# Performance work log

Hardware: AMD Instinct MI355X
Metric: run time of the kernel (lower is better)

Reference implementation:

```python
import jax, jax.numpy as jnp
import numpy as np

DIM = 768
HEADS = 12
HEAD_DIM = DIM // HEADS
TOPK = 100
SCALE = HEAD_DIM ** -0.5


def setup_inputs() -> dict:
    key = jax.random.key(0)
    k1, k2, k3, k4 = jax.random.split(key, 4)
    B, N = 8, 1024
    x = jax.random.normal(k1, (B, N, DIM), dtype=jnp.float32)
    # torch nn.Linear(dim, 3*dim, bias=False): store matmul-ready [in, out]
    w_qkv = jax.random.normal(k2, (DIM, 3 * DIM), dtype=jnp.float32) * (DIM ** -0.5)
    w_proj = jax.random.normal(k3, (DIM, DIM), dtype=jnp.float32) * (DIM ** -0.5)
    b_proj = jax.random.normal(k4, (DIM,), dtype=jnp.float32) * 0.01
    return {"x": x, "w_qkv": w_qkv, "w_proj": w_proj, "b_proj": b_proj}


def reference(x, w_qkv, w_proj, b_proj):
    B, N, C = x.shape
    qkv = (x @ w_qkv).reshape(B, N, 3, HEADS, HEAD_DIM)
    qkv = jnp.transpose(qkv, (2, 0, 3, 1, 4))  # [3, B, H, N, D]
    q, k, v = qkv[0], qkv[1], qkv[2]
    attn = jnp.einsum("bhnd,bhmd->bhnm", q, k) * SCALE  # [B, H, N, N]
    # top-k mask: keep entries >= k-th largest score per row (ties negligible
    # for continuous scores; matches torch topk+scatter mask semantics)
    kth = jax.lax.top_k(attn, TOPK)[0][..., -1:]  # [B, H, N, 1]
    attn = jnp.where(attn >= kth, attn, -jnp.inf)
    attn = jax.nn.softmax(attn, axis=-1)
    out = jnp.einsum("bhnm,bhmd->bhnd", attn, v)  # [B, H, N, D]
    out = jnp.transpose(out, (0, 2, 1, 3)).reshape(B, N, C)
    return out @ w_proj + b_proj
```

## Files before the change

### kernel.cpp

```cpp
#include <hip/hip_runtime.h>
#include <cstddef>

#define DIMC 768
#define HEADS 12
#define HEAD_DIM 64
#define TOPK 100
#define SCALE 0.125f
#define BATCH 8
#define SEQ 1024
#define RB 8
#define CAP 128
#define ATHR 512

typedef __attribute__((ext_vector_type(8))) __bf16 bf16x8;
typedef __attribute__((ext_vector_type(4))) float f32x4;
typedef unsigned short u16;

__device__ __forceinline__ unsigned mkey(float f) {
  unsigned u = __float_as_uint(f);
  return u ^ ((unsigned)((int)u >> 31) | 0x80000000u);
}

__device__ __forceinline__ void split_pack4(float4 f, uint2& ph, uint2& pl) {
  unsigned u0 = __float_as_uint(f.x), u1 = __float_as_uint(f.y);
  unsigned u2 = __float_as_uint(f.z), u3 = __float_as_uint(f.w);
  float r0 = f.x - __uint_as_float(u0 & 0xFFFF0000u);
  float r1 = f.y - __uint_as_float(u1 & 0xFFFF0000u);
  float r2 = f.z - __uint_as_float(u2 & 0xFFFF0000u);
  float r3 = f.w - __uint_as_float(u3 & 0xFFFF0000u);
  ph.x = (u0 >> 16) | (u1 & 0xFFFF0000u);
  ph.y = (u2 >> 16) | (u3 & 0xFFFF0000u);
  pl.x = (__float_as_uint(r0) >> 16) | (__float_as_uint(r1) & 0xFFFF0000u);
  pl.y = (__float_as_uint(r2) >> 16) | (__float_as_uint(r3) & 0xFFFF0000u);
}

template <int A_SPLIT, bool BIAS>
__global__ __launch_bounds__(256) void gemm_mfma_split(
    const float* __restrict__ Af,
    const u16* __restrict__ Ah_g, const u16* __restrict__ Al_g,
    const float* __restrict__ W,
    const float* __restrict__ bias, float* __restrict__ C,
    int M, int K, int N) {
  __shared__ u16 Ah[128][32], Al[128][32];
  __shared__ u16 Bh[128][32], Bl[128][32];

  const int t = threadIdx.x;
  const int w = t >> 6, l = t & 63;
  const int wr = w >> 1, wc = w & 1;
  const int row0 = blockIdx.y * 128, col0 = blockIdx.x * 128;
  const int fr = l & 15, fq = l >> 4;

  f32x4 acc[4][4];
#pragma unroll
  for (int i = 0; i < 4; ++i)
#pragma unroll
    for (int j = 0; j < 4; ++j) acc[i][j] = (f32x4){0.f, 0.f, 0.f, 0.f};

  const int a_row = t >> 1;
  const int a_k0 = (t & 1) * 16;
  const int w_col = t & 127;
  const int w_kh = (t >> 7) * 16;

  for (int k0 = 0; k0 < K; k0 += 32) {
    if constexpr (A_SPLIT == 0) {
      const float* ap = Af + (size_t)(row0 + a_row) * K + k0 + a_k0;
#pragma unroll
      for (int q = 0; q < 4; ++q) {
        float4 v = *(const float4*)(ap + q * 4);
        uint2 ph, pl;
        split_pack4(v, ph, pl);
        *(uint2*)&Ah[a_row][a_k0 + q * 4] = ph;
        *(uint2*)&Al[a_row][a_k0 + q * 4] = pl;
      }
    } else {
      const size_t off = (size_t)(row0 + a_row) * K + k0 + a_k0;
      *(uint4*)&Ah[a_row][a_k0] = *(const uint4*)(Ah_g + off);
      *(uint4*)&Ah[a_row][a_k0 + 8] = *(const uint4*)(Ah_g + off + 8);
      *(uint4*)&Al[a_row][a_k0] = *(const uint4*)(Al_g + off);
      *(uint4*)&Al[a_row][a_k0 + 8] = *(const uint4*)(Al_g + off + 8);
    }
    {
      const float* wp = W + (size_t)(k0 + w_kh) * N + col0 + w_col;
      float wv[16];
#pragma unroll
      for (int j = 0; j < 16; ++j) wv[j] = wp[(size_t)j * N];
#pragma unroll
      for (int g = 0; g < 4; ++g) {
        float4 v = make_float4(wv[g * 4], wv[g * 4 + 1], wv[g * 4 + 2], wv[g * 4 + 3]);
        uint2 ph, pl;
        split_pack4(v, ph, pl);
        *(uint2*)&Bh[w_col][w_kh + g * 4] = ph;
        *(uint2*)&Bl[w_col][w_kh + g * 4] = pl;
      }
    }
    __syncthreads();

    bf16x8 fah[4], fal[4], fbh[4], fbl[4];
#pragma unroll
    for (int mf = 0; mf < 4; ++mf) {
      fah[mf] = *(const bf16x8*)&Ah[wr * 64 + mf * 16 + fr][fq * 8];
      fal[mf] = *(const bf16x8*)&Al[wr * 64 + mf * 16 + fr][fq * 8];
    }
#pragma unroll
    for (int nf = 0; nf < 4; ++nf) {
      fbh[nf] = *(const bf16x8*)&Bh[wc * 64 + nf * 16 + fr][fq * 8];
      fbl[nf] = *(const bf16x8*)&Bl[wc * 64 + nf * 16 + fr][fq * 8];
    }
#pragma unroll
    for (int mf = 0; mf < 4; ++mf)
#pragma unroll
      for (int nf = 0; nf < 4; ++nf) {
        acc[mf][nf] = __builtin_amdgcn_mfma_f32_16x16x32_bf16(fah[mf], fbh[nf], acc[mf][nf], 0, 0, 0);
        acc[mf][nf] = __builtin_amdgcn_mfma_f32_16x16x32_bf16(fah[mf], fbl[nf], acc[mf][nf], 0, 0, 0);
        acc[mf][nf] = __builtin_amdgcn_mfma_f32_16x16x32_bf16(fal[mf], fbh[nf], acc[mf][nf], 0, 0, 0);
      }
    __syncthreads();
  }

#pragma unroll
  for (int mf = 0; mf < 4; ++mf) {
    const int r0 = row0 + wr * 64 + mf * 16 + fq * 4;
#pragma unroll
    for (int nf = 0; nf < 4; ++nf) {
      const int c = col0 + wc * 64 + nf * 16 + fr;
      float bb = 0.f;
      if (BIAS) bb = bias[c];
#pragma unroll
      for (int r = 0; r < 4; ++r)
        C[(size_t)(r0 + r) * N + c] = acc[mf][nf][r] + bb;
    }
  }
}

__global__ __launch_bounds__(ATHR) void attn_topk(
    const float* __restrict__ qkv,
    u16* __restrict__ aout_h, u16* __restrict__ aout_l) {
  __shared__ float s[RB][SEQ];
  __shared__ float qs[RB][HEAD_DIM];
  __shared__ unsigned short idxl[RB][CAP];
  __shared__ float pl[RB][CAP];

  const int t = threadIdx.x;
  const int n0 = blockIdx.x * RB;
  const int bh = blockIdx.y;
  const int b = bh / HEADS, h = bh - b * HEADS;
  const float* base = qkv + (size_t)b * SEQ * (3 * DIMC) + h * HEAD_DIM;

  {
    const int r = t >> 6, d = t & 63;
    qs[r][d] = base[(size_t)(n0 + r) * (3 * DIMC) + d] * SCALE;
  }
  __syncthreads();

  {
    const float* kp0 = base + DIMC + (size_t)t * (3 * DIMC);
    const float* kp1 = base + DIMC + (size_t)(t + 512) * (3 * DIMC);
    float a0[RB], a1[RB];
#pragma unroll
    for (int r = 0; r < RB; ++r) { a0[r] = 0.f; a1[r] = 0.f; }
#pragma unroll
    for (int d0 = 0; d0 < HEAD_DIM; d0 += 4) {
      float4 k0 = *(const float4*)(kp0 + d0);
      float4 k1 = *(const float4*)(kp1 + d0);
#pragma unroll
      for (int r = 0; r < RB; ++r) {
        float4 q4 = *(const float4*)&qs[r][d0];
        a0[r] += k0.x * q4.x + k0.y * q4.y + k0.z * q4.z + k0.w * q4.w;
        a1[r] += k1.x * q4.x + k1.y * q4.y + k1.z * q4.z + k1.w * q4.w;
      }
    }
#pragma unroll
    for (int r = 0; r < RB; ++r) {
      s[r][t] = a0[r];
      s[r][t + 512] = a1[r];
    }
  }
  __syncthreads();

  const int row = t >> 6, l = t & 63;

  float sc[16];
  unsigned ky[16];
#pragma unroll
  for (int j = 0; j < 16; ++j) sc[j] = s[row][l + 64 * j];
#pragma unroll
  for (int j = 0; j < 16; ++j) ky[j] = mkey(sc[j]);

  unsigned cur = 0u;
  for (int bit = 31; bit >= 0; --bit) {
    const unsigned T = cur | (1u << bit);
    int c = 0;
#pragma unroll
    for (int j = 0; j < 16; ++j) c += (ky[j] >= T) ? 1 : 0;
#pragma unroll
    for (int off = 32; off > 0; off >>= 1) c += __shfl_xor(c, off, 64);
    if (c >= TOPK) {
      cur = T;
      if (c == TOPK) break;
    }
  }

  float mx = sc[0];
#pragma unroll
  for (int j = 1; j < 16; ++j) mx = fmaxf(mx, sc[j]);
#pragma unroll
  for (int off = 32; off > 0; off >>= 1) mx = fmaxf(mx, __shfl_xor(mx, off, 64));

  float p[16];
  float sum = 0.f;
#pragma unroll
  for (int j = 0; j < 16; ++j) {
    const bool keep = ky[j] >= cur;
    const float e = __expf(sc[j] - mx);
    p[j] = keep ? e : 0.f;
    sum += p[j];
  }
#pragma unroll
  for (int off = 32; off > 0; off >>= 1) sum += __shfl_xor(sum, off, 64);
  const float rinv = 1.f / sum;

  unsigned cbase = 0;
#pragma unroll
  for (int j = 0; j < 16; ++j) {
    const bool keep = ky[j] >= cur;
    const unsigned long long mask = __ballot(keep);
    if (keep) {
      const unsigned pos = cbase + (unsigned)__popcll(mask & ((1ull << l) - 1ull));
      if (pos < CAP) {
        idxl[row][pos] = (unsigned short)(l + 64 * j);
        pl[row][pos] = p[j];
      }
    }
    cbase += (unsigned)__popcll(mask);
  }
  const unsigned cnt = cbase;

  {
    const float* vb = base + 2 * DIMC;
    float o = 0.f;
    if (cnt <= CAP) {
      unsigned j = 0;
      for (; j + 8 <= cnt; j += 8) {
        unsigned m[8]; float pv[8], vv[8];
#pragma unroll
        for (int q = 0; q < 8; ++q) m[q] = idxl[row][j + q];
#pragma unroll
        for (int q = 0; q < 8; ++q) pv[q] = pl[row][j + q];
#pragma unroll
        for (int q = 0; q < 8; ++q) vv[q] = vb[m[q] * (3u * DIMC) + l];
#pragma unroll
        for (int q = 0; q < 8; ++q) o = fmaf(pv[q], vv[q], o);
      }
      for (; j < cnt; ++j) {
        unsigned m = idxl[row][j];
        o = fmaf(pl[row][j], vb[m * (3u * DIMC) + l], o);
      }
    } else {
      for (int m = 0; m < SEQ; ++m) {
        float v = s[row][m];
        if (mkey(v) >= cur) o = fmaf(__expf(v - mx), vb[m * (3u * DIMC) + l], o);
      }
    }
    const float r = o * rinv;
    const unsigned u = __float_as_uint(r);
    const float rl = r - __uint_as_float(u & 0xFFFF0000u);
    const size_t idx = ((size_t)b * SEQ + n0 + row) * DIMC + h * HEAD_DIM + l;
    aout_h[idx] = (u16)(u >> 16);
    aout_l[idx] = (u16)(__float_as_uint(rl) >> 16);
  }
}

extern "C" void kernel_launch(void* const* d_in, const int* in_sizes, int n_in,
                              void* d_out, int out_size, void* d_ws, size_t ws_size,
                              hipStream_t stream) {
  (void)in_sizes; (void)n_in; (void)out_size; (void)ws_size;
  const float* x      = (const float*)d_in[0];
  const float* w_qkv  = (const float*)d_in[1];
  const float* w_proj = (const float*)d_in[2];
  const float* b_proj = (const float*)d_in[3];
  float* out = (float*)d_out;

  const int M = BATCH * SEQ;
  float* qkv = (float*)d_ws;
  u16* ah2 = (u16*)(qkv + (size_t)M * (3 * DIMC));
  u16* al2 = ah2 + (size_t)M * DIMC;

  dim3 g1((3 * DIMC) / 128, M / 128);
  gemm_mfma_split<0, false><<<g1, dim3(256), 0, stream>>>(
      x, nullptr, nullptr, w_qkv, nullptr, qkv, M, DIMC, 3 * DIMC);
  dim3 g2(SEQ / RB, BATCH * HEADS);
  attn_topk<<<g2, dim3(ATHR), 0, stream>>>(qkv, ah2, al2);
  dim3 g3(DIMC / 128, M / 128);
  gemm_mfma_split<1, true><<<g3, dim3(256), 0, stream>>>(
      nullptr, ah2, al2, w_proj, b_proj, out, M, DIMC, DIMC);
}
```

Baseline: 743.1 us.

## Compute QK^T scores with split-fp16 MFMA using K stored as fp16 hi/lo

The QKV GEMM epilogue now writes the K columns as fp16 hi/lo pairs packed into the row's byte space, and the attention kernel computes the score tile with 16x16x32 fp16 MFMAs (three-term split product) in place of scalar FMA dot products. Smaller changes go with it: the top-k bit search counts with ballot+popcount instead of shuffle reductions, the softmax pass is fused with compaction, and the V gather uses readfirstlane on the index. This targets the scalar-ALU and global-load cost of the QK^T stage. The risk is the split-fp16 precision in the scores, plus an MFMA tile of 16 rows where only 8 are valid, so half the MFMA work is discarded.

```diff
diff --git a/kernel.cpp b/kernel.cpp
--- a/kernel.cpp
+++ b/kernel.cpp
@@ -12,9 +12,12 @@
 #define CAP 128
 #define ATHR 512
 
+typedef _Float16 f16;
+typedef __attribute__((ext_vector_type(8))) _Float16 f16x8;
 typedef __attribute__((ext_vector_type(8))) __bf16 bf16x8;
 typedef __attribute__((ext_vector_type(4))) float f32x4;
 typedef unsigned short u16;
+
 
 __device__ __forceinline__ unsigned mkey(float f) {
   unsigned u = __float_as_uint(f);
@@ -34,7 +37,7 @@
   pl.y = (__float_as_uint(r2) >> 16) | (__float_as_uint(r3) & 0xFFFF0000u);
 }
 
-template <int A_SPLIT, bool BIAS>
+template <int A_SPLIT, bool BIAS, bool KSPLIT>
 __global__ __launch_bounds__(256) void gemm_mfma_split(
     const float* __restrict__ Af,
     const u16* __restrict__ Ah_g, const u16* __restrict__ Al_g,
@@ -117,17 +120,31 @@
     __syncthreads();
   }
 
+  const bool kzone = KSPLIT && (col0 >= 768) && (col0 < 1536);
 #pragma unroll
   for (int mf = 0; mf < 4; ++mf) {
     const int r0 = row0 + wr * 64 + mf * 16 + fq * 4;
 #pragma unroll
     for (int nf = 0; nf < 4; ++nf) {
       const int c = col0 + wc * 64 + nf * 16 + fr;
-      float bb = 0.f;
-      if (BIAS) bb = bias[c];
-#pragma unroll
-      for (int r = 0; r < 4; ++r)
-        C[(size_t)(r0 + r) * N + c] = acc[mf][nf][r] + bb;
+      if (kzone) {
+        f16* cb = (f16*)C;
+#pragma unroll
+        for (int r = 0; r < 4; ++r) {
+          float v = acc[mf][nf][r];
+          f16 hh = (f16)v;
+          f16 hl = (f16)(v - (float)hh);
+          f16* rp = cb + (size_t)(r0 + r) * 4608;
+          rp[c + 768] = hh;
+          rp[c + 1536] = hl;
+        }
+      } else {
+        float bb = 0.f;
+        if (BIAS) bb = bias[c];
+#pragma unroll
+        for (int r = 0; r < 4; ++r)
+          C[(size_t)(r0 + r) * N + c] = acc[mf][nf][r] + bb;
+      }
     }
   }
 }
@@ -136,7 +153,8 @@
     const float* __restrict__ qkv,
     u16* __restrict__ aout_h, u16* __restrict__ aout_l) {
   __shared__ float s[RB][SEQ];
-  __shared__ float qs[RB][HEAD_DIM];
+  __shared__ __align__(16) f16 Qh[16][64];
+  __shared__ __align__(16) f16 Ql[16][64];
   __shared__ unsigned short idxl[RB][CAP];
   __shared__ float pl[RB][CAP];
 
@@ -144,40 +162,50 @@
   const int n0 = blockIdx.x * RB;
   const int bh = blockIdx.y;
   const int b = bh / HEADS, h = bh - b * HEADS;
-  const float* base = qkv + (size_t)b * SEQ * (3 * DIMC) + h * HEAD_DIM;
+  const float* qf = qkv + (size_t)b * SEQ * (3 * DIMC);
+  const f16* kb = (const f16*)qkv + (size_t)b * SEQ * 4608 + 1536 + h * 64;
 
   {
     const int r = t >> 6, d = t & 63;
-    qs[r][d] = base[(size_t)(n0 + r) * (3 * DIMC) + d] * SCALE;
+    float q = qf[(size_t)(n0 + r) * (3 * DIMC) + h * 64 + d] * SCALE;
+    f16 hh = (f16)q;
+    Qh[r][d] = hh;
+    Ql[r][d] = (f16)(q - (float)hh);
   }
   __syncthreads();
 
+  const int w = t >> 6, l = t & 63;
+  const int fr = l & 15, fq = l >> 4;
+
   {
-    const float* kp0 = base + DIMC + (size_t)t * (3 * DIMC);
-    const float* kp1 = base + DIMC + (size_t)(t + 512) * (3 * DIMC);
-    float a0[RB], a1[RB];
-#pragma unroll
-    for (int r = 0; r < RB; ++r) { a0[r] = 0.f; a1[r] = 0.f; }
-#pragma unroll
-    for (int d0 = 0; d0 < HEAD_DIM; d0 += 4) {
-      float4 k0 = *(const float4*)(kp0 + d0);
-      float4 k1 = *(const float4*)(kp1 + d0);
-#pragma unroll
-      for (int r = 0; r < RB; ++r) {
-        float4 q4 = *(const float4*)&qs[r][d0];
-        a0[r] += k0.x * q4.x + k0.y * q4.y + k0.z * q4.z + k0.w * q4.w;
-        a1[r] += k1.x * q4.x + k1.y * q4.y + k1.z * q4.z + k1.w * q4.w;
-      }
-    }
-#pragma unroll
-    for (int r = 0; r < RB; ++r) {
-      s[r][t] = a0[r];
-      s[r][t + 512] = a1[r];
+    f16x8 ah0 = *(const f16x8*)&Qh[fr][fq * 8];
+    f16x8 ah1 = *(const f16x8*)&Qh[fr][32 + fq * 8];
+    f16x8 al0 = *(const f16x8*)&Ql[fr][fq * 8];
+    f16x8 al1 = *(const f16x8*)&Ql[fr][32 + fq * 8];
+#pragma unroll
+    for (int i = 0; i < 8; ++i) {
+      const int tile = w * 8 + i;
+      const f16* kr = kb + (size_t)(tile * 16 + fr) * 4608;
+      f16x8 bh0 = *(const f16x8*)(kr + fq * 8);
+      f16x8 bh1 = *(const f16x8*)(kr + 32 + fq * 8);
+      f16x8 bl0 = *(const f16x8*)(kr + 768 + fq * 8);
+      f16x8 bl1 = *(const f16x8*)(kr + 768 + 32 + fq * 8);
+      f32x4 acc = (f32x4){0.f, 0.f, 0.f, 0.f};
+      acc = __builtin_amdgcn_mfma_f32_16x16x32_f16(ah0, bh0, acc, 0, 0, 0);
+      acc = __builtin_amdgcn_mfma_f32_16x16x32_f16(ah0, bl0, acc, 0, 0, 0);
+      acc = __builtin_amdgcn_mfma_f32_16x16x32_f16(al0, bh0, acc, 0, 0, 0);
+      acc = __builtin_amdgcn_mfma_f32_16x16x32_f16(ah1, bh1, acc, 0, 0, 0);
+      acc = __builtin_amdgcn_mfma_f32_16x16x32_f16(ah1, bl1, acc, 0, 0, 0);
+      acc = __builtin_amdgcn_mfma_f32_16x16x32_f16(al1, bh1, acc, 0, 0, 0);
+      if (fq < 2) {
+#pragma unroll
+        for (int r = 0; r < 4; ++r) s[fq * 4 + r][tile * 16 + fr] = acc[r];
+      }
     }
   }
   __syncthreads();
 
-  const int row = t >> 6, l = t & 63;
+  const int row = w;
 
   float sc[16];
   unsigned ky[16];
@@ -191,9 +219,8 @@
     const unsigned T = cur | (1u << bit);
     int c = 0;
 #pragma unroll
-    for (int j = 0; j < 16; ++j) c += (ky[j] >= T) ? 1 : 0;
-#pragma unroll
-    for (int off = 32; off > 0; off >>= 1) c += __shfl_xor(c, off, 64);
+    for (int j = 0; j < 16; ++j)
+      c += (int)__popcll(__ballot(ky[j] >= T));
     if (c >= TOPK) {
       cur = T;
       if (c == TOPK) break;
@@ -206,65 +233,58 @@
 #pragma unroll
   for (int off = 32; off > 0; off >>= 1) mx = fmaxf(mx, __shfl_xor(mx, off, 64));
 
-  float p[16];
   float sum = 0.f;
+  unsigned cbase = 0;
 #pragma unroll
   for (int j = 0; j < 16; ++j) {
     const bool keep = ky[j] >= cur;
-    const float e = __expf(sc[j] - mx);
-    p[j] = keep ? e : 0.f;
-    sum += p[j];
-  }
-#pragma unroll
-  for (int off = 32; off > 0; off >>= 1) sum += __shfl_xor(sum, off, 64);
-  const float rinv = 1.f / sum;
-
-  unsigned cbase = 0;
-#pragma unroll
-  for (int j = 0; j < 16; ++j) {
-    const bool keep = ky[j] >= cur;
+    const float e = keep ? __expf(sc[j] - mx) : 0.f;
+    sum += e;
     const unsigned long long mask = __ballot(keep);
     if (keep) {
       const unsigned pos = cbase + (unsigned)__popcll(mask & ((1ull << l) - 1ull));
       if (pos < CAP) {
         idxl[row][pos] = (unsigned short)(l + 64 * j);
-        pl[row][pos] = p[j];
+        pl[row][pos] = e;
       }
     }
     cbase += (unsigned)__popcll(mask);
   }
   const unsigned cnt = cbase;
+#pragma unroll
+  for (int off = 32; off > 0; off >>= 1) sum += __shfl_xor(sum, off, 64);
+  const float rinv = 1.f / sum;
 
   {
-    const float* vb = base + 2 * DIMC;
+    const float* vb = qf + 1536 + h * 64;
     float o = 0.f;
     if (cnt <= CAP) {
       unsigned j = 0;
       for (; j + 8 <= cnt; j += 8) {
-        unsigned m[8]; float pv[8], vv[8];
-#pragma unroll
-        for (int q = 0; q < 8; ++q) m[q] = idxl[row][j + q];
-#pragma unroll
-        for (int q = 0; q < 8; ++q) pv[q] = pl[row][j + q];
-#pragma unroll
-        for (int q = 0; q < 8; ++q) vv[q] = vb[m[q] * (3u * DIMC) + l];
+        float pv[8], vv[8];
+#pragma unroll
+        for (int q = 0; q < 8; ++q) {
+          const int m = __builtin_amdgcn_readfirstlane((int)idxl[row][j + q]);
+          vv[q] = vb[(size_t)m * (3 * DIMC) + l];
+          pv[q] = pl[row][j + q];
+        }
 #pragma unroll
         for (int q = 0; q < 8; ++q) o = fmaf(pv[q], vv[q], o);
       }
       for (; j < cnt; ++j) {
-        unsigned m = idxl[row][j];
-        o = fmaf(pl[row][j], vb[m * (3u * DIMC) + l], o);
+        const int m = __builtin_amdgcn_readfirstlane((int)idxl[row][j]);
+        o = fmaf(pl[row][j], vb[(size_t)m * (3 * DIMC) + l], o);
       }
     } else {
       for (int m = 0; m < SEQ; ++m) {
         float v = s[row][m];
-        if (mkey(v) >= cur) o = fmaf(__expf(v - mx), vb[m * (3u * DIMC) + l], o);
+        if (mkey(v) >= cur) o = fmaf(__expf(v - mx), vb[(size_t)m * (3 * DIMC) + l], o);
       }
     }
     const float r = o * rinv;
     const unsigned u = __float_as_uint(r);
     const float rl = r - __uint_as_float(u & 0xFFFF0000u);
-    const size_t idx = ((size_t)b * SEQ + n0 + row) * DIMC + h * HEAD_DIM + l;
+    const size_t idx = ((size_t)b * SEQ + n0 + row) * DIMC + h * 64 + l;
     aout_h[idx] = (u16)(u >> 16);
     aout_l[idx] = (u16)(__float_as_uint(rl) >> 16);
   }
@@ -286,11 +306,11 @@
   u16* al2 = ah2 + (size_t)M * DIMC;
 
   dim3 g1((3 * DIMC) / 128, M / 128);
-  gemm_mfma_split<0, false><<<g1, dim3(256), 0, stream>>>(
+  gemm_mfma_split<0, false, true><<<g1, dim3(256), 0, stream>>>(
       x, nullptr, nullptr, w_qkv, nullptr, qkv, M, DIMC, 3 * DIMC);
   dim3 g2(SEQ / RB, BATCH * HEADS);
   attn_topk<<<g2, dim3(ATHR), 0, stream>>>(qkv, ah2, al2);
   dim3 g3(DIMC / 128, M / 128);
-  gemm_mfma_split<1, true><<<g3, dim3(256), 0, stream>>>(
+  gemm_mfma_split<1, true, false><<<g3, dim3(256), 0, stream>>>(
       nullptr, ah2, al2, w_proj, b_proj, out, M, DIMC, DIMC);
 }
```

New measurement: 692.2 us. 1.07x faster.
